# Performance work log

Hardware: AMD Instinct MI355X
Metric: run time of the kernel (lower is better)

Reference implementation:

```python
import jax, jax.numpy as jnp
import numpy as np

DIM = 256
HEADS = 8
WS = 7


def _ln(x, w, b, eps=1e-5):
    m = x.mean(-1, keepdims=True)
    v = x.var(-1, keepdims=True)
    return (x - m) / jnp.sqrt(v + eps) * w + b


def setup_inputs() -> dict:
    key = jax.random.key(0)
    ks = jax.random.split(key, 6)
    d = DIM
    s = 0.02
    return {
        "x": jax.random.normal(ks[0], (8, d, 224, 224), jnp.float32),
        "norm1_w": jnp.ones((d,), jnp.float32),
        "norm1_b": jnp.zeros((d,), jnp.float32),
        "in_proj_w": jax.random.normal(ks[1], (3 * d, d), jnp.float32) * s,
        "in_proj_b": jnp.zeros((3 * d,), jnp.float32),
        "out_proj_w": jax.random.normal(ks[2], (d, d), jnp.float32) * s,
        "out_proj_b": jnp.zeros((d,), jnp.float32),
        "norm2_w": jnp.ones((d,), jnp.float32),
        "norm2_b": jnp.zeros((d,), jnp.float32),
        "mlp_w1": jax.random.normal(ks[3], (4 * d, d), jnp.float32) * s,
        "mlp_b1": jnp.zeros((4 * d,), jnp.float32),
        "mlp_w2": jax.random.normal(ks[4], (d, 4 * d), jnp.float32) * s,
        "mlp_b2": jnp.zeros((d,), jnp.float32),
    }


def reference(x, norm1_w, norm1_b, in_proj_w, in_proj_b, out_proj_w, out_proj_b,
              norm2_w, norm2_b, mlp_w1, mlp_b1, mlp_w2, mlp_b2):
    B, C, H, W = x.shape
    ws, h = WS, HEADS
    dh = C // h
    pad_h = (ws - H % ws) % ws
    pad_w = (ws - W % ws) % ws
    xp = jnp.pad(x, ((0, 0), (0, 0), (0, pad_h), (0, pad_w)))
    Hp, Wp = xp.shape[2], xp.shape[3]
    # window partition: (B,C,Hp,Wp) -> (B*nWh*nWw, ws*ws, C)
    win = xp.reshape(B, C, Hp // ws, ws, Wp // ws, ws)
    win = win.transpose(0, 2, 4, 3, 5, 1).reshape(-1, ws * ws, C)
    win = _ln(win, norm1_w, norm1_b)  # residual stream is the NORMED windows (as in source)
    # multi-head self-attention (torch nn.MultiheadAttention semantics)
    qkv = win @ in_proj_w.T + in_proj_b
    q, k, v = jnp.split(qkv, 3, axis=-1)
    N, L, _ = win.shape
    q = q.reshape(N, L, h, dh)
    k = k.reshape(N, L, h, dh)
    v = v.reshape(N, L, h, dh)
    scores = jnp.einsum('nlhd,nmhd->nhlm', q, k) / jnp.sqrt(jnp.float32(dh))
    att = jax.nn.softmax(scores, axis=-1)
    o = jnp.einsum('nhlm,nmhd->nlhd', att, v).reshape(N, L, C)
    o = o @ out_proj_w.T + out_proj_b
    win = win + o
    # MLP with exact GELU (torch nn.GELU default)
    hmid = jax.nn.gelu(_ln(win, norm2_w, norm2_b) @ mlp_w1.T + mlp_b1, approximate=False)
    win = win + (hmid @ mlp_w2.T + mlp_b2)
    # window reverse: (N, ws*ws, C) -> (B, C, Hp, Wp)
    xo = win.reshape(B, Hp // ws, Wp // ws, ws, ws, C)
    xo = xo.transpose(0, 5, 1, 3, 2, 4).reshape(B, C, Hp, Wp)
    return xo[:, :, :H, :W]
```

## Files before the change

### kernel.cpp

```cpp
#include <hip/hip_runtime.h>
#include <hip/hip_bf16.h>
#include <math.h>

#define DEVI __device__ __forceinline__
typedef __attribute__((ext_vector_type(8))) short bf16x8;
typedef __attribute__((ext_vector_type(4))) float f32x4;

#define MFMA(a, b, c) __builtin_amdgcn_mfma_f32_16x16x32_bf16((a), (b), (c), 0, 0, 0)

DEVI short f2bf(float f) {
    unsigned u = __builtin_bit_cast(unsigned, f);
    return (short)((u + 0x7FFFu + ((u >> 16) & 1u)) >> 16);
}
DEVI float bf2f(short s) {
    unsigned u = ((unsigned)(unsigned short)s) << 16;
    return __builtin_bit_cast(float, u);
}
DEVI int swz(int row, int cb, int ld) { return row * ld + (cb ^ ((row & 7) << 4)); }
DEVI bf16x8 gload_bf8(const float* p) {
    const f32x4* q = (const f32x4*)p;
    f32x4 a = q[0], b = q[1];
    bf16x8 r;
    r[0] = f2bf(a[0]); r[1] = f2bf(a[1]); r[2] = f2bf(a[2]); r[3] = f2bf(a[3]);
    r[4] = f2bf(b[0]); r[5] = f2bf(b[1]); r[6] = f2bf(b[2]); r[7] = f2bf(b[3]);
    return r;
}

__global__ void prep_frag(const float* __restrict__ s, short* __restrict__ d,
                          int kd32, int n) {
    int i = blockIdx.x * 256 + threadIdx.x;
    if (i >= n) return;
    int lane = i & 63;
    int gt = i >> 6;
    int g = gt % kd32, tile = gt / kd32;
    int j = tile * 16 + (lane & 15);
    int k0 = g * 32 + (lane >> 4) * 8;
    int Kd = kd32 * 32;
    bf16x8 o = gload_bf8(s + (size_t)j * Kd + k0);
    *(bf16x8*)(d + (size_t)i * 8) = o;
}

__global__ __launch_bounds__(512, 2) void swin_attn(
    const float* __restrict__ x,
    const float* __restrict__ n1w, const float* __restrict__ n1b,
    const short* __restrict__ WqB, const float* __restrict__ Bq,
    const short* __restrict__ WoB, const float* __restrict__ Bo,
    short* __restrict__ Rws)
{
    extern __shared__ __align__(16) char smem[];
    constexpr int OB = 0, CQ = 25088, CK = 31360, CV = 37632, SW = 50176, ST = 75264;

    const int bid = blockIdx.x;
    const int b = bid >> 10, wh = (bid >> 5) & 31, w7 = bid & 31;
    const int tid = threadIdx.x, wv = tid >> 6, lane = tid & 63;
    const int lg = lane >> 4, l15 = lane & 15;
    const int c0 = wv * 32 + l15;
    const f32x4 z = {0.f, 0.f, 0.f, 0.f};

    {
        float* sX = (float*)smem;
        const float* xb = x + (size_t)b * (256 * 224 * 224);
        for (int i = tid; i < 256 * 49; i += 512) {
            int c = i / 49, l = i - c * 49;
            int hh = wh * 7 + l / 7, ww = w7 * 7 + (l % 7);
            sX[i] = xb[((size_t)c * 224 + hh) * 224 + ww];
        }
    }
    __syncthreads();
    {
        const int l = tid >> 3, s = tid & 7;
        if (l < 49) {
            const float* sX = (const float*)smem;
            float sum = 0.f, sq = 0.f;
            for (int ii = 0; ii < 32; ++ii) {
                int c = s * 32 + ((ii + tid) & 31);
                float v = sX[c * 49 + l];
                sum += v; sq += v * v;
            }
#pragma unroll
            for (int m = 1; m < 8; m <<= 1) { sum += __shfl_xor(sum, m); sq += __shfl_xor(sq, m); }
            if (s == 0) {
                float mean = sum * (1.f / 256.f);
                ((float*)(smem + ST))[l * 2] = mean;
                ((float*)(smem + ST))[l * 2 + 1] = rsqrtf(sq * (1.f / 256.f) - mean * mean + 1e-5f);
            }
        }
    }
    __syncthreads();
    {
        const float* sX = (const float*)smem;
        const float* st = (const float*)(smem + ST);
        float w0 = n1w[c0], b0 = n1b[c0], w1 = n1w[c0 + 16], b1 = n1b[c0 + 16];
#pragma unroll
        for (int ct = 0; ct < 2; ++ct)
#pragma unroll
        for (int mt = 0; mt < 4; ++mt)
#pragma unroll
        for (int r = 0; r < 4; ++r) {
            int row = mt * 16 + lg * 4 + r, col = c0 + ct * 16;
            if (row < 49) {
                float v = (sX[col * 49 + row] - st[row * 2]) * st[row * 2 + 1] * (ct ? w1 : w0) + (ct ? b1 : b0);
                *(short*)(smem + SW + swz(row, col * 2, 512)) = f2bf(v);
            }
        }
    }
    __syncthreads();

    const int grp = wv >> 2, mts = wv & 3;
    int arow = mts * 16 + l15; if (arow > 48) arow = 48;
#pragma unroll 1
    for (int hp = 0; hp < 4; ++hp) {
#pragma unroll 1
        for (int sub = 0; sub < 2; ++sub) {
            if (sub == 0 || wv < 4) {
                const int t = sub ? (8 + wv) : wv;
                const int part = t >> 2, tt = t & 3;
                const int lc = tt * 16 + l15;
                const int jw = part * 256 + hp * 64 + lc;
                const int wtile = part * 16 + hp * 4 + tt;
                f32x4 a0 = z, a1 = z, a2 = z, a3 = z;
#pragma unroll
                for (int kk = 0; kk < 8; ++kk) {
                    bf16x8 bw = *(const bf16x8*)(WqB + (((size_t)(wtile * 8 + kk) * 64 + lane) << 3));
                    const int cb = kk * 64 + lg * 16;
                    bf16x8 f0 = *(const bf16x8*)(smem + SW + swz(l15, cb, 512));
                    bf16x8 f1 = *(const bf16x8*)(smem + SW + swz(16 + l15, cb, 512));
                    bf16x8 f2 = *(const bf16x8*)(smem + SW + swz(32 + l15, cb, 512));
                    bf16x8 f3 = *(const bf16x8*)(smem + SW + swz(48, cb, 512));
                    a0 = MFMA(f0, bw, a0); a1 = MFMA(f1, bw, a1);
                    a2 = MFMA(f2, bw, a2); a3 = MFMA(f3, bw, a3);
                }
                const float bias = Bq[jw];
                if (part < 2) {
                    char* base = smem + (part ? CK : CQ);
#pragma unroll
                    for (int mt = 0; mt < 4; ++mt) {
                        f32x4 av = (mt == 0) ? a0 : (mt == 1) ? a1 : (mt == 2) ? a2 : a3;
#pragma unroll
                        for (int r = 0; r < 4; ++r) {
                            int row = mt * 16 + lg * 4 + r;
                            if (row < 49) *(short*)(base + swz(row, lc * 2, 128)) = f2bf(av[r] + bias);
                        }
                    }
                } else {
#pragma unroll
                    for (int mt = 0; mt < 4; ++mt) {
                        f32x4 av = (mt == 0) ? a0 : (mt == 1) ? a1 : (mt == 2) ? a2 : a3;
#pragma unroll
                        for (int r = 0; r < 4; ++r) {
                            int row = mt * 16 + lg * 4 + r;
                            *(short*)(smem + CV + swz(lc, row * 2, 128)) = f2bf(av[r] + bias);
                        }
                    }
                }
            }
        }
        __syncthreads();
        const int hb = grp * 64 + lg * 16;
        f32x4 s0 = z, s1 = z, s2 = z, s3 = z;
        {
            bf16x8 qa = *(const bf16x8*)(smem + CQ + swz(arow, hb, 128));
            bf16x8 k0 = *(const bf16x8*)(smem + CK + swz(l15, hb, 128));
            bf16x8 k1 = *(const bf16x8*)(smem + CK + swz(16 + l15, hb, 128));
            bf16x8 k2 = *(const bf16x8*)(smem + CK + swz(32 + l15, hb, 128));
            bf16x8 k3 = *(const bf16x8*)(smem + CK + swz(48, hb, 128));
            s0 = MFMA(qa, k0, s0); s1 = MFMA(qa, k1, s1);
            s2 = MFMA(qa, k2, s2); s3 = MFMA(qa, k3, s3);
        }
        const float scale = 0.17677669529663687f;
        float pr[4][4];
#pragma unroll
        for (int rj = 0; rj < 4; ++rj) {
            float v0 = s0[rj] * scale, v1 = s1[rj] * scale;
            float v2 = s2[rj] * scale, v3 = s3[rj] * scale;
            const int c3 = 48 + l15;
            float mx = fmaxf(fmaxf(v0, v1), v2);
            if (c3 < 49) mx = fmaxf(mx, v3);
#pragma unroll
            for (int mm = 1; mm < 16; mm <<= 1) mx = fmaxf(mx, __shfl_xor(mx, mm));
            float e0 = __expf(v0 - mx), e1 = __expf(v1 - mx), e2 = __expf(v2 - mx);
            float e3 = (c3 < 49) ? __expf(v3 - mx) : 0.f;
            float sm = e0 + e1 + e2 + e3;
#pragma unroll
            for (int mm = 1; mm < 16; mm <<= 1) sm += __shfl_xor(sm, mm);
            float inv = 1.f / sm;
            pr[rj][0] = e0 * inv; pr[rj][1] = e1 * inv;
            pr[rj][2] = e2 * inv; pr[rj][3] = e3 * inv;
        }
        __syncthreads();
        char* satt = smem + CQ + grp * 6272;
#pragma unroll
        for (int rj = 0; rj < 4; ++rj) {
            int row = mts * 16 + lg * 4 + rj;
            if (row < 49) {
                *(short*)(satt + swz(row, l15 * 2, 128)) = f2bf(pr[rj][0]);
                *(short*)(satt + swz(row, (16 + l15) * 2, 128)) = f2bf(pr[rj][1]);
                *(short*)(satt + swz(row, (32 + l15) * 2, 128)) = f2bf(pr[rj][2]);
                *(short*)(satt + swz(row, (48 + l15) * 2, 128)) = f2bf(pr[rj][3]);
            }
        }
        __syncthreads();
        f32x4 o0 = z, o1 = z;
#pragma unroll
        for (int kk = 0; kk < 2; ++kk) {
            const int kb = kk * 64 + lg * 16;
            bf16x8 pa  = *(const bf16x8*)(satt + swz(arow, kb, 128));
            bf16x8 vb0 = *(const bf16x8*)(smem + CV + swz(grp * 32 + l15, kb, 128));
            bf16x8 vb1 = *(const bf16x8*)(smem + CV + swz(grp * 32 + 16 + l15, kb, 128));
            o0 = MFMA(pa, vb0, o0); o1 = MFMA(pa, vb1, o1);
        }
#pragma unroll
        for (int nt = 0; nt < 2; ++nt) {
            f32x4 ov = nt ? o1 : o0;
#pragma unroll
            for (int r = 0; r < 4; ++r) {
                int row = mts * 16 + lg * 4 + r;
                if (row < 49) {
                    int col = hp * 64 + grp * 32 + nt * 16 + l15;
                    *(short*)(smem + OB + swz(row, col * 2, 512)) = f2bf(ov[r]);
                }
            }
        }
        __syncthreads();
    }

#pragma unroll 1
    for (int ct = 0; ct < 2; ++ct) {
        const int j = c0 + ct * 16;
        const int wtile = wv * 2 + ct;
        f32x4 a0 = z, a1 = z, a2 = z, a3 = z;
#pragma unroll
        for (int kk = 0; kk < 8; ++kk) {
            bf16x8 bw = *(const bf16x8*)(WoB + (((size_t)(wtile * 8 + kk) * 64 + lane) << 3));
            const int cb = kk * 64 + lg * 16;
            bf16x8 f0 = *(const bf16x8*)(smem + OB + swz(l15, cb, 512));
            bf16x8 f1 = *(const bf16x8*)(smem + OB + swz(16 + l15, cb, 512));
            bf16x8 f2 = *(const bf16x8*)(smem + OB + swz(32 + l15, cb, 512));
            bf16x8 f3 = *(const bf16x8*)(smem + OB + swz(48, cb, 512));
            a0 = MFMA(f0, bw, a0); a1 = MFMA(f1, bw, a1);
            a2 = MFMA(f2, bw, a2); a3 = MFMA(f3, bw, a3);
        }
        const float bias = Bo[j];
#pragma unroll
        for (int mt = 0; mt < 4; ++mt) {
            f32x4 av = (mt == 0) ? a0 : (mt == 1) ? a1 : (mt == 2) ? a2 : a3;
#pragma unroll
            for (int r = 0; r < 4; ++r) {
                int row = mt * 16 + lg * 4 + r;
                if (row < 49) {
                    short* p = (short*)(smem + SW + swz(row, j * 2, 512));
                    *p = f2bf(bf2f(*p) + av[r] + bias);
                }
            }
        }
    }
    __syncthreads();
    {
        for (int i = tid; i < 49 * 32; i += 512) {
            int row = i >> 5, c8 = (i & 31) * 8;
            bf16x8 v = *(const bf16x8*)(smem + SW + swz(row, c8 * 2, 512));
            *(bf16x8*)(Rws + ((size_t)bid * 49 + row) * 256 + c8) = v;
        }
    }
}

__global__ __launch_bounds__(1024, 1) void mlp_kernel(
    const short* __restrict__ Rws,
    const float* __restrict__ n2w, const float* __restrict__ n2b,
    const short* __restrict__ W1B, const float* __restrict__ B1,
    const short* __restrict__ W2B, const float* __restrict__ B2,
    float* __restrict__ out)
{
    extern __shared__ __align__(16) char smem[];
    constexpr int HB = 65536;
    const int tile = blockIdx.x;
    const int tid = threadIdx.x, wv = tid >> 6, lane = tid & 63;
    const int lg = lane >> 4, l15 = lane & 15;
    const int wm = wv >> 3, wn = wv & 7;
    const int r0 = wm * 64;
    const f32x4 z = {0.f, 0.f, 0.f, 0.f};

#pragma unroll
    for (int it = 0; it < 4; ++it) {
        int e = it * 1024 + tid;
        int row = e >> 5, c8 = (e & 31) * 8;
        bf16x8 v = *(const bf16x8*)(Rws + ((size_t)tile * 128 + row) * 256 + c8);
        *(bf16x8*)(smem + swz(row, c8 * 2, 512)) = v;
    }
    __syncthreads();
    {
        const int row = tid >> 3, sub = tid & 7;
        bf16x8 vv[4];
        float sum = 0.f, sq = 0.f;
#pragma unroll
        for (int ii = 0; ii < 4; ++ii) {
            vv[ii] = *(const bf16x8*)(smem + swz(row, (sub * 32 + ii * 8) * 2, 512));
#pragma unroll
            for (int j = 0; j < 8; ++j) { float f = bf2f(vv[ii][j]); sum += f; sq += f * f; }
        }
#pragma unroll
        for (int m = 1; m < 8; m <<= 1) { sum += __shfl_xor(sum, m); sq += __shfl_xor(sq, m); }
        const float mean = sum * (1.f / 256.f);
        const float rstd = rsqrtf(sq * (1.f / 256.f) - mean * mean + 1e-5f);
#pragma unroll
        for (int ii = 0; ii < 4; ++ii) {
            f32x4 w0 = *(const f32x4*)(n2w + sub * 32 + ii * 8);
            f32x4 w1 = *(const f32x4*)(n2w + sub * 32 + ii * 8 + 4);
            f32x4 b0 = *(const f32x4*)(n2b + sub * 32 + ii * 8);
            f32x4 b1 = *(const f32x4*)(n2b + sub * 32 + ii * 8 + 4);
            bf16x8 o;
#pragma unroll
            for (int j = 0; j < 8; ++j) {
                float wj = (j < 4) ? w0[j] : w1[j - 4];
                float bj = (j < 4) ? b0[j] : b1[j - 4];
                o[j] = f2bf((bf2f(vv[ii][j]) - mean) * rstd * wj + bj);
            }
            *(bf16x8*)(smem + swz(row, (sub * 32 + ii * 8) * 2, 512)) = o;
        }
    }
    __syncthreads();

    f32x4 macc[8];
#pragma unroll
    for (int i = 0; i < 8; ++i) macc[i] = z;

#pragma unroll 1
    for (int c = 0; c < 8; ++c) {
        f32x4 g1[4];
#pragma unroll
        for (int i = 0; i < 4; ++i) g1[i] = z;
#pragma unroll
        for (int kk = 0; kk < 8; ++kk) {
            const int cb = kk * 64 + lg * 16;
            bf16x8 a0 = *(const bf16x8*)(smem + swz(r0 + l15,      cb, 512));
            bf16x8 a1 = *(const bf16x8*)(smem + swz(r0 + 16 + l15, cb, 512));
            bf16x8 a2 = *(const bf16x8*)(smem + swz(r0 + 32 + l15, cb, 512));
            bf16x8 a3 = *(const bf16x8*)(smem + swz(r0 + 48 + l15, cb, 512));
            const int t = c * 8 + wn;
            bf16x8 wf = *(const bf16x8*)(W1B + (((size_t)(t * 8 + kk) * 64 + lane) << 3));
            g1[0] = MFMA(a0, wf, g1[0]);
            g1[1] = MFMA(a1, wf, g1[1]);
            g1[2] = MFMA(a2, wf, g1[2]);
            g1[3] = MFMA(a3, wf, g1[3]);
        }
        __syncthreads();
        {
            const int hc = wn * 16 + l15;
            const float bias = B1[c * 128 + hc];
#pragma unroll
            for (int mt = 0; mt < 4; ++mt) {
#pragma unroll
                for (int r = 0; r < 4; ++r) {
                    int row = r0 + mt * 16 + lg * 4 + r;
                    float v = g1[mt][r] + bias;
                    float g = v / (1.f + __expf(-v * (1.595769122f + 0.071354816f * v * v)));
                    *(short*)(smem + HB + swz(row, hc * 2, 256)) = f2bf(g);
                }
            }
        }
        __syncthreads();
#pragma unroll
        for (int ks = 0; ks < 4; ++ks) {
            const int cb = ks * 64 + lg * 16;
            bf16x8 h0 = *(const bf16x8*)(smem + HB + swz(r0 + l15,      cb, 256));
            bf16x8 h1 = *(const bf16x8*)(smem + HB + swz(r0 + 16 + l15, cb, 256));
            bf16x8 h2 = *(const bf16x8*)(smem + HB + swz(r0 + 32 + l15, cb, 256));
            bf16x8 h3 = *(const bf16x8*)(smem + HB + swz(r0 + 48 + l15, cb, 256));
#pragma unroll
            for (int ct = 0; ct < 2; ++ct) {
                const int t = wn * 2 + ct;
                const int g = c * 4 + ks;
                bf16x8 wf = *(const bf16x8*)(W2B + (((size_t)(t * 32 + g) * 64 + lane) << 3));
                macc[ct * 4 + 0] = MFMA(h0, wf, macc[ct * 4 + 0]);
                macc[ct * 4 + 1] = MFMA(h1, wf, macc[ct * 4 + 1]);
                macc[ct * 4 + 2] = MFMA(h2, wf, macc[ct * 4 + 2]);
                macc[ct * 4 + 3] = MFMA(h3, wf, macc[ct * 4 + 3]);
            }
        }
    }
    __syncthreads();
    float* stg = (float*)smem;
#pragma unroll 1
    for (int half = 0; half < 2; ++half) {
        if (wm == half) {
#pragma unroll
            for (int ct = 0; ct < 2; ++ct) {
                const int col = wn * 32 + ct * 16 + l15;
                const float b2v = B2[col];
#pragma unroll
                for (int mt = 0; mt < 4; ++mt) {
#pragma unroll
                    for (int r = 0; r < 4; ++r) {
                        int rl = mt * 16 + lg * 4 + r;
                        size_t t = (size_t)tile * 128 + half * 64 + rl;
                        float rv = bf2f(Rws[t * 256 + col]);
                        stg[rl * 260 + col] = rv + macc[ct * 4 + mt][r] + b2v;
                    }
                }
            }
        }
        __syncthreads();
        for (int i = tid; i < 64 * 256; i += 1024) {
            int cc = i >> 6, rl = i & 63;
            int t = tile * 128 + half * 64 + rl;
            int win = t / 49, l = t - win * 49;
            int b = win >> 10, wh = (win >> 5) & 31, w7 = win & 31;
            out[((size_t)(b * 256 + cc) * 224 + wh * 7 + l / 7) * 224 + w7 * 7 + (l % 7)] =
                stg[rl * 260 + cc];
        }
        __syncthreads();
    }
}

extern "C" void kernel_launch(void* const* d_in, const int* in_sizes, int n_in,
                              void* d_out, int out_size, void* d_ws, size_t ws_size,
                              hipStream_t stream) {
    const float* x   = (const float*)d_in[0];
    const float* n1w = (const float*)d_in[1];
    const float* n1b = (const float*)d_in[2];
    const float* Wq  = (const float*)d_in[3];
    const float* Bq  = (const float*)d_in[4];
    const float* Wo  = (const float*)d_in[5];
    const float* Bo  = (const float*)d_in[6];
    const float* n2w = (const float*)d_in[7];
    const float* n2b = (const float*)d_in[8];
    const float* W1  = (const float*)d_in[9];
    const float* B1  = (const float*)d_in[10];
    const float* W2  = (const float*)d_in[11];
    const float* B2  = (const float*)d_in[12];
    float* out = (float*)d_out;
    (void)in_sizes; (void)n_in; (void)out_size; (void)ws_size;

    short* wsp = (short*)d_ws;
    short* WqF = wsp;
    short* WoF = wsp + 196608;
    short* W1F = wsp + 262144;
    short* W2F = wsp + 524288;
    short* Rws = wsp + 786432;

    prep_frag<<<96, 256, 0, stream>>>(Wq, WqF, 8, 24576);
    prep_frag<<<32, 256, 0, stream>>>(Wo, WoF, 8, 8192);
    prep_frag<<<128, 256, 0, stream>>>(W1, W1F, 8, 32768);
    prep_frag<<<128, 256, 0, stream>>>(W2, W2F, 32, 32768);

    swin_attn<<<8192, 512, 76288, stream>>>(x, n1w, n1b, WqF, Bq, WoF, Bo, Rws);
    mlp_kernel<<<3136, 1024, 98304, stream>>>(Rws, n2w, n2b, W1F, B1, W2F, B2, out);
}
```

Baseline: 2.253 ms.

## Rebalance QKV work across waves, drop attention barriers, double MLP hidden chunk

In the attention kernel, QKV projection work is redistributed so all 8 waves do one Q/K tile plus half a V tile, replacing the two-pass schedule where only half the waves ran the second pass. The attention probabilities move to a separate per-group area in OB, which removes two __syncthreads per head pair. The outputs for the last two head pairs are kept in registers and written after the loop. The MLP kernel processes 256-wide hidden chunks in 4 iterations instead of 128-wide in 8, halving the barriers there. That costs more shared memory (131072 bytes) and accumulator registers, which may reduce occupancy.

```diff
diff --git a/kernel.cpp b/kernel.cpp
--- a/kernel.cpp
+++ b/kernel.cpp
@@ -108,50 +108,63 @@
 
     const int grp = wv >> 2, mts = wv & 3;
     int arow = mts * 16 + l15; if (arow > 48) arow = 48;
+    char* satt = smem + OB + 256 + grp * 128;
+    f32x4 osave[4];
+
 #pragma unroll 1
     for (int hp = 0; hp < 4; ++hp) {
-#pragma unroll 1
-        for (int sub = 0; sub < 2; ++sub) {
-            if (sub == 0 || wv < 4) {
-                const int t = sub ? (8 + wv) : wv;
-                const int part = t >> 2, tt = t & 3;
-                const int lc = tt * 16 + l15;
-                const int jw = part * 256 + hp * 64 + lc;
-                const int wtile = part * 16 + hp * 4 + tt;
-                f32x4 a0 = z, a1 = z, a2 = z, a3 = z;
-#pragma unroll
-                for (int kk = 0; kk < 8; ++kk) {
-                    bf16x8 bw = *(const bf16x8*)(WqB + (((size_t)(wtile * 8 + kk) * 64 + lane) << 3));
-                    const int cb = kk * 64 + lg * 16;
-                    bf16x8 f0 = *(const bf16x8*)(smem + SW + swz(l15, cb, 512));
-                    bf16x8 f1 = *(const bf16x8*)(smem + SW + swz(16 + l15, cb, 512));
-                    bf16x8 f2 = *(const bf16x8*)(smem + SW + swz(32 + l15, cb, 512));
-                    bf16x8 f3 = *(const bf16x8*)(smem + SW + swz(48, cb, 512));
-                    a0 = MFMA(f0, bw, a0); a1 = MFMA(f1, bw, a1);
-                    a2 = MFMA(f2, bw, a2); a3 = MFMA(f3, bw, a3);
-                }
-                const float bias = Bq[jw];
-                if (part < 2) {
-                    char* base = smem + (part ? CK : CQ);
-#pragma unroll
-                    for (int mt = 0; mt < 4; ++mt) {
-                        f32x4 av = (mt == 0) ? a0 : (mt == 1) ? a1 : (mt == 2) ? a2 : a3;
-#pragma unroll
-                        for (int r = 0; r < 4; ++r) {
-                            int row = mt * 16 + lg * 4 + r;
-                            if (row < 49) *(short*)(base + swz(row, lc * 2, 128)) = f2bf(av[r] + bias);
-                        }
-                    }
-                } else {
-#pragma unroll
-                    for (int mt = 0; mt < 4; ++mt) {
-                        f32x4 av = (mt == 0) ? a0 : (mt == 1) ? a1 : (mt == 2) ? a2 : a3;
-#pragma unroll
-                        for (int r = 0; r < 4; ++r) {
-                            int row = mt * 16 + lg * 4 + r;
-                            *(short*)(smem + CV + swz(lc, row * 2, 128)) = f2bf(av[r] + bias);
-                        }
-                    }
+        {
+            const int part = wv >> 2, tt = wv & 3;
+            const int lc = tt * 16 + l15;
+            const int jw = part * 256 + hp * 64 + lc;
+            const int wtile = part * 16 + hp * 4 + tt;
+            f32x4 a0 = z, a1 = z, a2 = z, a3 = z;
+#pragma unroll
+            for (int kk = 0; kk < 8; ++kk) {
+                bf16x8 bw = *(const bf16x8*)(WqB + (((size_t)(wtile * 8 + kk) * 64 + lane) << 3));
+                const int cb = kk * 64 + lg * 16;
+                bf16x8 f0 = *(const bf16x8*)(smem + SW + swz(l15, cb, 512));
+                bf16x8 f1 = *(const bf16x8*)(smem + SW + swz(16 + l15, cb, 512));
+                bf16x8 f2 = *(const bf16x8*)(smem + SW + swz(32 + l15, cb, 512));
+                bf16x8 f3 = *(const bf16x8*)(smem + SW + swz(48, cb, 512));
+                a0 = MFMA(f0, bw, a0); a1 = MFMA(f1, bw, a1);
+                a2 = MFMA(f2, bw, a2); a3 = MFMA(f3, bw, a3);
+            }
+            const float bias = Bq[jw];
+            char* base = smem + (part ? CK : CQ);
+#pragma unroll
+            for (int mt = 0; mt < 4; ++mt) {
+                f32x4 av = (mt == 0) ? a0 : (mt == 1) ? a1 : (mt == 2) ? a2 : a3;
+#pragma unroll
+                for (int r = 0; r < 4; ++r) {
+                    int row = mt * 16 + lg * 4 + r;
+                    if (row < 49) *(short*)(base + swz(row, lc * 2, 128)) = f2bf(av[r] + bias);
+                }
+            }
+        }
+        {
+            const int tt = wv & 3, hf = wv >> 2;
+            const int lc = tt * 16 + l15;
+            const int jw = 512 + hp * 64 + lc;
+            const int wtile = 32 + hp * 4 + tt;
+            f32x4 a0 = z, a1 = z;
+#pragma unroll
+            for (int kk = 0; kk < 8; ++kk) {
+                bf16x8 bw = *(const bf16x8*)(WqB + (((size_t)(wtile * 8 + kk) * 64 + lane) << 3));
+                const int cb = kk * 64 + lg * 16;
+                bf16x8 f0 = *(const bf16x8*)(smem + SW + swz(hf * 32 + l15, cb, 512));
+                bf16x8 f1 = hf ? *(const bf16x8*)(smem + SW + swz(48, cb, 512))
+                               : *(const bf16x8*)(smem + SW + swz(16 + l15, cb, 512));
+                a0 = MFMA(f0, bw, a0); a1 = MFMA(f1, bw, a1);
+            }
+            const float bias = Bq[jw];
+#pragma unroll
+            for (int mt = 0; mt < 2; ++mt) {
+                f32x4 av = mt ? a1 : a0;
+#pragma unroll
+                for (int r = 0; r < 4; ++r) {
+                    int row = (hf * 2 + mt) * 16 + lg * 4 + r;
+                    *(short*)(smem + CV + swz(lc, row * 2, 128)) = f2bf(av[r] + bias);
                 }
             }
         }
@@ -168,7 +181,6 @@
             s2 = MFMA(qa, k2, s2); s3 = MFMA(qa, k3, s3);
         }
         const float scale = 0.17677669529663687f;
-        float pr[4][4];
 #pragma unroll
         for (int rj = 0; rj < 4; ++rj) {
             float v0 = s0[rj] * scale, v1 = s1[rj] * scale;
@@ -184,45 +196,55 @@
 #pragma unroll
             for (int mm = 1; mm < 16; mm <<= 1) sm += __shfl_xor(sm, mm);
             float inv = 1.f / sm;
-            pr[rj][0] = e0 * inv; pr[rj][1] = e1 * inv;
-            pr[rj][2] = e2 * inv; pr[rj][3] = e3 * inv;
-        }
-        __syncthreads();
-        char* satt = smem + CQ + grp * 6272;
-#pragma unroll
-        for (int rj = 0; rj < 4; ++rj) {
             int row = mts * 16 + lg * 4 + rj;
             if (row < 49) {
-                *(short*)(satt + swz(row, l15 * 2, 128)) = f2bf(pr[rj][0]);
-                *(short*)(satt + swz(row, (16 + l15) * 2, 128)) = f2bf(pr[rj][1]);
-                *(short*)(satt + swz(row, (32 + l15) * 2, 128)) = f2bf(pr[rj][2]);
-                *(short*)(satt + swz(row, (48 + l15) * 2, 128)) = f2bf(pr[rj][3]);
-            }
-        }
-        __syncthreads();
+                *(short*)(satt + swz(row, l15 * 2, 512)) = f2bf(e0 * inv);
+                *(short*)(satt + swz(row, (16 + l15) * 2, 512)) = f2bf(e1 * inv);
+                *(short*)(satt + swz(row, (32 + l15) * 2, 512)) = f2bf(e2 * inv);
+                *(short*)(satt + swz(row, (48 + l15) * 2, 512)) = f2bf(e3 * inv);
+            }
+        }
         f32x4 o0 = z, o1 = z;
 #pragma unroll
         for (int kk = 0; kk < 2; ++kk) {
             const int kb = kk * 64 + lg * 16;
-            bf16x8 pa  = *(const bf16x8*)(satt + swz(arow, kb, 128));
+            bf16x8 pa  = *(const bf16x8*)(satt + swz(arow, kb, 512));
             bf16x8 vb0 = *(const bf16x8*)(smem + CV + swz(grp * 32 + l15, kb, 128));
             bf16x8 vb1 = *(const bf16x8*)(smem + CV + swz(grp * 32 + 16 + l15, kb, 128));
             o0 = MFMA(pa, vb0, o0); o1 = MFMA(pa, vb1, o1);
         }
-#pragma unroll
-        for (int nt = 0; nt < 2; ++nt) {
-            f32x4 ov = nt ? o1 : o0;
-#pragma unroll
-            for (int r = 0; r < 4; ++r) {
-                int row = mts * 16 + lg * 4 + r;
-                if (row < 49) {
-                    int col = hp * 64 + grp * 32 + nt * 16 + l15;
-                    *(short*)(smem + OB + swz(row, col * 2, 512)) = f2bf(ov[r]);
-                }
-            }
-        }
-        __syncthreads();
-    }
+        if (hp < 2) {
+#pragma unroll
+            for (int nt = 0; nt < 2; ++nt) {
+                f32x4 ov = nt ? o1 : o0;
+#pragma unroll
+                for (int r = 0; r < 4; ++r) {
+                    int row = mts * 16 + lg * 4 + r;
+                    if (row < 49) {
+                        int col = hp * 64 + grp * 32 + nt * 16 + l15;
+                        *(short*)(smem + OB + swz(row, col * 2, 512)) = f2bf(ov[r]);
+                    }
+                }
+            }
+        } else if (hp == 2) { osave[0] = o0; osave[1] = o1; }
+        else                { osave[2] = o0; osave[3] = o1; }
+        __syncthreads();
+    }
+#pragma unroll
+    for (int h2 = 0; h2 < 2; ++h2)
+#pragma unroll
+    for (int nt = 0; nt < 2; ++nt) {
+        f32x4 ov = osave[h2 * 2 + nt];
+#pragma unroll
+        for (int r = 0; r < 4; ++r) {
+            int row = mts * 16 + lg * 4 + r;
+            if (row < 49) {
+                int col = (2 + h2) * 64 + grp * 32 + nt * 16 + l15;
+                *(short*)(smem + OB + swz(row, col * 2, 512)) = f2bf(ov[r]);
+            }
+        }
+    }
+    __syncthreads();
 
 #pragma unroll 1
     for (int ct = 0; ct < 2; ++ct) {
@@ -325,10 +347,10 @@
     for (int i = 0; i < 8; ++i) macc[i] = z;
 
 #pragma unroll 1
-    for (int c = 0; c < 8; ++c) {
-        f32x4 g1[4];
-#pragma unroll
-        for (int i = 0; i < 4; ++i) g1[i] = z;
+    for (int c = 0; c < 4; ++c) {
+        f32x4 g1[8];
+#pragma unroll
+        for (int i = 0; i < 8; ++i) g1[i] = z;
 #pragma unroll
         for (int kk = 0; kk < 8; ++kk) {
             const int cb = kk * 64 + lg * 16;
@@ -336,41 +358,45 @@
             bf16x8 a1 = *(const bf16x8*)(smem + swz(r0 + 16 + l15, cb, 512));
             bf16x8 a2 = *(const bf16x8*)(smem + swz(r0 + 32 + l15, cb, 512));
             bf16x8 a3 = *(const bf16x8*)(smem + swz(r0 + 48 + l15, cb, 512));
-            const int t = c * 8 + wn;
-            bf16x8 wf = *(const bf16x8*)(W1B + (((size_t)(t * 8 + kk) * 64 + lane) << 3));
-            g1[0] = MFMA(a0, wf, g1[0]);
-            g1[1] = MFMA(a1, wf, g1[1]);
-            g1[2] = MFMA(a2, wf, g1[2]);
-            g1[3] = MFMA(a3, wf, g1[3]);
-        }
-        __syncthreads();
-        {
-            const int hc = wn * 16 + l15;
-            const float bias = B1[c * 128 + hc];
+#pragma unroll
+            for (int ct = 0; ct < 2; ++ct) {
+                const int t = c * 16 + wn * 2 + ct;
+                bf16x8 wf = *(const bf16x8*)(W1B + (((size_t)(t * 8 + kk) * 64 + lane) << 3));
+                g1[ct * 4 + 0] = MFMA(a0, wf, g1[ct * 4 + 0]);
+                g1[ct * 4 + 1] = MFMA(a1, wf, g1[ct * 4 + 1]);
+                g1[ct * 4 + 2] = MFMA(a2, wf, g1[ct * 4 + 2]);
+                g1[ct * 4 + 3] = MFMA(a3, wf, g1[ct * 4 + 3]);
+            }
+        }
+        __syncthreads();
+#pragma unroll
+        for (int ct = 0; ct < 2; ++ct) {
+            const int hc = wn * 32 + ct * 16 + l15;
+            const float bias = B1[c * 256 + hc];
 #pragma unroll
             for (int mt = 0; mt < 4; ++mt) {
 #pragma unroll
                 for (int r = 0; r < 4; ++r) {
                     int row = r0 + mt * 16 + lg * 4 + r;
-                    float v = g1[mt][r] + bias;
+                    float v = g1[ct * 4 + mt][r] + bias;
                     float g = v / (1.f + __expf(-v * (1.595769122f + 0.071354816f * v * v)));
-                    *(short*)(smem + HB + swz(row, hc * 2, 256)) = f2bf(g);
-                }
-            }
-        }
-        __syncthreads();
-#pragma unroll
-        for (int ks = 0; ks < 4; ++ks) {
+                    *(short*)(smem + HB + swz(row, hc * 2, 512)) = f2bf(g);
+                }
+            }
+        }
+        __syncthreads();
+#pragma unroll
+        for (int ks = 0; ks < 8; ++ks) {
             const int cb = ks * 64 + lg * 16;
-            bf16x8 h0 = *(const bf16x8*)(smem + HB + swz(r0 + l15,      cb, 256));
-            bf16x8 h1 = *(const bf16x8*)(smem + HB + swz(r0 + 16 + l15, cb, 256));
-            bf16x8 h2 = *(const bf16x8*)(smem + HB + swz(r0 + 32 + l15, cb, 256));
-            bf16x8 h3 = *(const bf16x8*)(smem + HB + swz(r0 + 48 + l15, cb, 256));
+            bf16x8 h0 = *(const bf16x8*)(smem + HB + swz(r0 + l15,      cb, 512));
+            bf16x8 h1 = *(const bf16x8*)(smem + HB + swz(r0 + 16 + l15, cb, 512));
+            bf16x8 h2 = *(const bf16x8*)(smem + HB + swz(r0 + 32 + l15, cb, 512));
+            bf16x8 h3 = *(const bf16x8*)(smem + HB + swz(r0 + 48 + l15, cb, 512));
 #pragma unroll
             for (int ct = 0; ct < 2; ++ct) {
-                const int t = wn * 2 + ct;
-                const int g = c * 4 + ks;
-                bf16x8 wf = *(const bf16x8*)(W2B + (((size_t)(t * 32 + g) * 64 + lane) << 3));
+                const int t2 = wn * 2 + ct;
+                const int g = c * 8 + ks;
+                bf16x8 wf = *(const bf16x8*)(W2B + (((size_t)(t2 * 32 + g) * 64 + lane) << 3));
                 macc[ct * 4 + 0] = MFMA(h0, wf, macc[ct * 4 + 0]);
                 macc[ct * 4 + 1] = MFMA(h1, wf, macc[ct * 4 + 1]);
                 macc[ct * 4 + 2] = MFMA(h2, wf, macc[ct * 4 + 2]);
@@ -444,5 +470,5 @@
     prep_frag<<<128, 256, 0, stream>>>(W2, W2F, 32, 32768);
 
     swin_attn<<<8192, 512, 76288, stream>>>(x, n1w, n1b, WqF, Bq, WoF, Bo, Rws);
-    mlp_kernel<<<3136, 1024, 98304, stream>>>(Rws, n2w, n2b, W1F, B1, W2F, B2, out);
-}
+    mlp_kernel<<<3136, 1024, 131072, stream>>>(Rws, n2w, n2b, W1F, B1, W2F, B2, out);
+}
```

Result: slower. 2.991 ms (+32.7%).

## Double-buffer MLP hidden tile and widen LDS swizzle for 512-byte rows

Applied to the files above, without the earlier changes.

The MLP hidden-activation buffer alternates between two LDS regions by chunk parity. This lets the barrier between the first GEMM and the GELU write be removed, since writers no longer overwrite data other waves may still be reading. The XOR swizzle for 512- and 256-byte row buffers now uses 16 row phases instead of 8, to cut LDS bank conflicts on the wide fragment loads. The MLP kernel's dynamic LDS grows from 96 KB to 128 KB, which may lower occupancy.

```diff
diff --git a/kernel.cpp b/kernel.cpp
--- a/kernel.cpp
+++ b/kernel.cpp
@@ -16,7 +16,8 @@
     unsigned u = ((unsigned)(unsigned short)s) << 16;
     return __builtin_bit_cast(float, u);
 }
-DEVI int swz(int row, int cb, int ld) { return row * ld + (cb ^ ((row & 7) << 4)); }
+DEVI int swz8(int row, int cb, int ld) { return row * ld + (cb ^ ((row & 7) << 4)); }
+DEVI int swz16(int row, int cb, int ld) { return row * ld + (cb ^ ((row & 15) << 4)); }
 DEVI bf16x8 gload_bf8(const float* p) {
     const f32x4* q = (const f32x4*)p;
     f32x4 a = q[0], b = q[1];
@@ -100,7 +101,7 @@
             int row = mt * 16 + lg * 4 + r, col = c0 + ct * 16;
             if (row < 49) {
                 float v = (sX[col * 49 + row] - st[row * 2]) * st[row * 2 + 1] * (ct ? w1 : w0) + (ct ? b1 : b0);
-                *(short*)(smem + SW + swz(row, col * 2, 512)) = f2bf(v);
+                *(short*)(smem + SW + swz16(row, col * 2, 512)) = f2bf(v);
             }
         }
     }
@@ -123,10 +124,10 @@
                 for (int kk = 0; kk < 8; ++kk) {
                     bf16x8 bw = *(const bf16x8*)(WqB + (((size_t)(wtile * 8 + kk) * 64 + lane) << 3));
                     const int cb = kk * 64 + lg * 16;
-                    bf16x8 f0 = *(const bf16x8*)(smem + SW + swz(l15, cb, 512));
-                    bf16x8 f1 = *(const bf16x8*)(smem + SW + swz(16 + l15, cb, 512));
-                    bf16x8 f2 = *(const bf16x8*)(smem + SW + swz(32 + l15, cb, 512));
-                    bf16x8 f3 = *(const bf16x8*)(smem + SW + swz(48, cb, 512));
+                    bf16x8 f0 = *(const bf16x8*)(smem + SW + swz16(l15, cb, 512));
+                    bf16x8 f1 = *(const bf16x8*)(smem + SW + swz16(16 + l15, cb, 512));
+                    bf16x8 f2 = *(const bf16x8*)(smem + SW + swz16(32 + l15, cb, 512));
+                    bf16x8 f3 = *(const bf16x8*)(smem + SW + swz16(48, cb, 512));
                     a0 = MFMA(f0, bw, a0); a1 = MFMA(f1, bw, a1);
                     a2 = MFMA(f2, bw, a2); a3 = MFMA(f3, bw, a3);
                 }
@@ -139,7 +140,7 @@
 #pragma unroll
                         for (int r = 0; r < 4; ++r) {
                             int row = mt * 16 + lg * 4 + r;
-                            if (row < 49) *(short*)(base + swz(row, lc * 2, 128)) = f2bf(av[r] + bias);
+                            if (row < 49) *(short*)(base + swz8(row, lc * 2, 128)) = f2bf(av[r] + bias);
                         }
                     }
                 } else {
@@ -149,7 +150,7 @@
 #pragma unroll
                         for (int r = 0; r < 4; ++r) {
                             int row = mt * 16 + lg * 4 + r;
-                            *(short*)(smem + CV + swz(lc, row * 2, 128)) = f2bf(av[r] + bias);
+                            *(short*)(smem + CV + swz8(lc, row * 2, 128)) = f2bf(av[r] + bias);
                         }
                     }
                 }
@@ -159,11 +160,11 @@
         const int hb = grp * 64 + lg * 16;
         f32x4 s0 = z, s1 = z, s2 = z, s3 = z;
         {
-            bf16x8 qa = *(const bf16x8*)(smem + CQ + swz(arow, hb, 128));
-            bf16x8 k0 = *(const bf16x8*)(smem + CK + swz(l15, hb, 128));
-            bf16x8 k1 = *(const bf16x8*)(smem + CK + swz(16 + l15, hb, 128));
-            bf16x8 k2 = *(const bf16x8*)(smem + CK + swz(32 + l15, hb, 128));
-            bf16x8 k3 = *(const bf16x8*)(smem + CK + swz(48, hb, 128));
+            bf16x8 qa = *(const bf16x8*)(smem + CQ + swz8(arow, hb, 128));
+            bf16x8 k0 = *(const bf16x8*)(smem + CK + swz8(l15, hb, 128));
+            bf16x8 k1 = *(const bf16x8*)(smem + CK + swz8(16 + l15, hb, 128));
+            bf16x8 k2 = *(const bf16x8*)(smem + CK + swz8(32 + l15, hb, 128));
+            bf16x8 k3 = *(const bf16x8*)(smem + CK + swz8(48, hb, 128));
             s0 = MFMA(qa, k0, s0); s1 = MFMA(qa, k1, s1);
             s2 = MFMA(qa, k2, s2); s3 = MFMA(qa, k3, s3);
         }
@@ -193,10 +194,10 @@
         for (int rj = 0; rj < 4; ++rj) {
             int row = mts * 16 + lg * 4 + rj;
             if (row < 49) {
-                *(short*)(satt + swz(row, l15 * 2, 128)) = f2bf(pr[rj][0]);
-                *(short*)(satt + swz(row, (16 + l15) * 2, 128)) = f2bf(pr[rj][1]);
-                *(short*)(satt + swz(row, (32 + l15) * 2, 128)) = f2bf(pr[rj][2]);
-                *(short*)(satt + swz(row, (48 + l15) * 2, 128)) = f2bf(pr[rj][3]);
+                *(short*)(satt + swz8(row, l15 * 2, 128)) = f2bf(pr[rj][0]);
+                *(short*)(satt + swz8(row, (16 + l15) * 2, 128)) = f2bf(pr[rj][1]);
+                *(short*)(satt + swz8(row, (32 + l15) * 2, 128)) = f2bf(pr[rj][2]);
+                *(short*)(satt + swz8(row, (48 + l15) * 2, 128)) = f2bf(pr[rj][3]);
             }
         }
         __syncthreads();
@@ -204,9 +205,9 @@
 #pragma unroll
         for (int kk = 0; kk < 2; ++kk) {
             const int kb = kk * 64 + lg * 16;
-            bf16x8 pa  = *(const bf16x8*)(satt + swz(arow, kb, 128));
-            bf16x8 vb0 = *(const bf16x8*)(smem + CV + swz(grp * 32 + l15, kb, 128));
-            bf16x8 vb1 = *(const bf16x8*)(smem + CV + swz(grp * 32 + 16 + l15, kb, 128));
+            bf16x8 pa  = *(const bf16x8*)(satt + swz8(arow, kb, 128));
+            bf16x8 vb0 = *(const bf16x8*)(smem + CV + swz8(grp * 32 + l15, kb, 128));
+            bf16x8 vb1 = *(const bf16x8*)(smem + CV + swz8(grp * 32 + 16 + l15, kb, 128));
             o0 = MFMA(pa, vb0, o0); o1 = MFMA(pa, vb1, o1);
         }
 #pragma unroll
@@ -217,7 +218,7 @@
                 int row = mts * 16 + lg * 4 + r;
                 if (row < 49) {
                     int col = hp * 64 + grp * 32 + nt * 16 + l15;
-                    *(short*)(smem + OB + swz(row, col * 2, 512)) = f2bf(ov[r]);
+                    *(short*)(smem + OB + swz16(row, col * 2, 512)) = f2bf(ov[r]);
                 }
             }
         }
@@ -233,10 +234,10 @@
         for (int kk = 0; kk < 8; ++kk) {
             bf16x8 bw = *(const bf16x8*)(WoB + (((size_t)(wtile * 8 + kk) * 64 + lane) << 3));
             const int cb = kk * 64 + lg * 16;
-            bf16x8 f0 = *(const bf16x8*)(smem + OB + swz(l15, cb, 512));
-            bf16x8 f1 = *(const bf16x8*)(smem + OB + swz(16 + l15, cb, 512));
-            bf16x8 f2 = *(const bf16x8*)(smem + OB + swz(32 + l15, cb, 512));
-            bf16x8 f3 = *(const bf16x8*)(smem + OB + swz(48, cb, 512));
+            bf16x8 f0 = *(const bf16x8*)(smem + OB + swz16(l15, cb, 512));
+            bf16x8 f1 = *(const bf16x8*)(smem + OB + swz16(16 + l15, cb, 512));
+            bf16x8 f2 = *(const bf16x8*)(smem + OB + swz16(32 + l15, cb, 512));
+            bf16x8 f3 = *(const bf16x8*)(smem + OB + swz16(48, cb, 512));
             a0 = MFMA(f0, bw, a0); a1 = MFMA(f1, bw, a1);
             a2 = MFMA(f2, bw, a2); a3 = MFMA(f3, bw, a3);
         }
@@ -248,7 +249,7 @@
             for (int r = 0; r < 4; ++r) {
                 int row = mt * 16 + lg * 4 + r;
                 if (row < 49) {
-                    short* p = (short*)(smem + SW + swz(row, j * 2, 512));
+                    short* p = (short*)(smem + SW + swz16(row, j * 2, 512));
                     *p = f2bf(bf2f(*p) + av[r] + bias);
                 }
             }
@@ -258,7 +259,7 @@
     {
         for (int i = tid; i < 49 * 32; i += 512) {
             int row = i >> 5, c8 = (i & 31) * 8;
-            bf16x8 v = *(const bf16x8*)(smem + SW + swz(row, c8 * 2, 512));
+            bf16x8 v = *(const bf16x8*)(smem + SW + swz16(row, c8 * 2, 512));
             *(bf16x8*)(Rws + ((size_t)bid * 49 + row) * 256 + c8) = v;
         }
     }
@@ -272,7 +273,7 @@
     float* __restrict__ out)
 {
     extern __shared__ __align__(16) char smem[];
-    constexpr int HB = 65536;
+    constexpr int HB0 = 65536, HB1 = 98304;
     const int tile = blockIdx.x;
     const int tid = threadIdx.x, wv = tid >> 6, lane = tid & 63;
     const int lg = lane >> 4, l15 = lane & 15;
@@ -285,7 +286,7 @@
         int e = it * 1024 + tid;
         int row = e >> 5, c8 = (e & 31) * 8;
         bf16x8 v = *(const bf16x8*)(Rws + ((size_t)tile * 128 + row) * 256 + c8);
-        *(bf16x8*)(smem + swz(row, c8 * 2, 512)) = v;
+        *(bf16x8*)(smem + swz16(row, c8 * 2, 512)) = v;
     }
     __syncthreads();
     {
@@ -294,7 +295,7 @@
         float sum = 0.f, sq = 0.f;
 #pragma unroll
         for (int ii = 0; ii < 4; ++ii) {
-            vv[ii] = *(const bf16x8*)(smem + swz(row, (sub * 32 + ii * 8) * 2, 512));
+            vv[ii] = *(const bf16x8*)(smem + swz16(row, (sub * 32 + ii * 8) * 2, 512));
 #pragma unroll
             for (int j = 0; j < 8; ++j) { float f = bf2f(vv[ii][j]); sum += f; sq += f * f; }
         }
@@ -315,7 +316,7 @@
                 float bj = (j < 4) ? b0[j] : b1[j - 4];
                 o[j] = f2bf((bf2f(vv[ii][j]) - mean) * rstd * wj + bj);
             }
-            *(bf16x8*)(smem + swz(row, (sub * 32 + ii * 8) * 2, 512)) = o;
+            *(bf16x8*)(smem + swz16(row, (sub * 32 + ii * 8) * 2, 512)) = o;
         }
     }
     __syncthreads();
@@ -326,16 +327,17 @@
 
 #pragma unroll 1
     for (int c = 0; c < 8; ++c) {
+        char* HB = smem + ((c & 1) ? HB1 : HB0);
         f32x4 g1[4];
 #pragma unroll
         for (int i = 0; i < 4; ++i) g1[i] = z;
 #pragma unroll
         for (int kk = 0; kk < 8; ++kk) {
             const int cb = kk * 64 + lg * 16;
-            bf16x8 a0 = *(const bf16x8*)(smem + swz(r0 + l15,      cb, 512));
-            bf16x8 a1 = *(const bf16x8*)(smem + swz(r0 + 16 + l15, cb, 512));
-            bf16x8 a2 = *(const bf16x8*)(smem + swz(r0 + 32 + l15, cb, 512));
-            bf16x8 a3 = *(const bf16x8*)(smem + swz(r0 + 48 + l15, cb, 512));
+            bf16x8 a0 = *(const bf16x8*)(smem + swz16(r0 + l15,      cb, 512));
+            bf16x8 a1 = *(const bf16x8*)(smem + swz16(r0 + 16 + l15, cb, 512));
+            bf16x8 a2 = *(const bf16x8*)(smem + swz16(r0 + 32 + l15, cb, 512));
+            bf16x8 a3 = *(const bf16x8*)(smem + swz16(r0 + 48 + l15, cb, 512));
             const int t = c * 8 + wn;
             bf16x8 wf = *(const bf16x8*)(W1B + (((size_t)(t * 8 + kk) * 64 + lane) << 3));
             g1[0] = MFMA(a0, wf, g1[0]);
@@ -343,7 +345,6 @@
             g1[2] = MFMA(a2, wf, g1[2]);
             g1[3] = MFMA(a3, wf, g1[3]);
         }
-        __syncthreads();
         {
             const int hc = wn * 16 + l15;
             const float bias = B1[c * 128 + hc];
@@ -354,7 +355,7 @@
                     int row = r0 + mt * 16 + lg * 4 + r;
                     float v = g1[mt][r] + bias;
                     float g = v / (1.f + __expf(-v * (1.595769122f + 0.071354816f * v * v)));
-                    *(short*)(smem + HB + swz(row, hc * 2, 256)) = f2bf(g);
+                    *(short*)(HB + swz16(row, hc * 2, 256)) = f2bf(g);
                 }
             }
         }
@@ -362,15 +363,15 @@
 #pragma unroll
         for (int ks = 0; ks < 4; ++ks) {
             const int cb = ks * 64 + lg * 16;
-            bf16x8 h0 = *(const bf16x8*)(smem + HB + swz(r0 + l15,      cb, 256));
-            bf16x8 h1 = *(const bf16x8*)(smem + HB + swz(r0 + 16 + l15, cb, 256));
-            bf16x8 h2 = *(const bf16x8*)(smem + HB + swz(r0 + 32 + l15, cb, 256));
-            bf16x8 h3 = *(const bf16x8*)(smem + HB + swz(r0 + 48 + l15, cb, 256));
+            bf16x8 h0 = *(const bf16x8*)(HB + swz16(r0 + l15,      cb, 256));
+            bf16x8 h1 = *(const bf16x8*)(HB + swz16(r0 + 16 + l15, cb, 256));
+            bf16x8 h2 = *(const bf16x8*)(HB + swz16(r0 + 32 + l15, cb, 256));
+            bf16x8 h3 = *(const bf16x8*)(HB + swz16(r0 + 48 + l15, cb, 256));
 #pragma unroll
             for (int ct = 0; ct < 2; ++ct) {
-                const int t = wn * 2 + ct;
+                const int t2 = wn * 2 + ct;
                 const int g = c * 4 + ks;
-                bf16x8 wf = *(const bf16x8*)(W2B + (((size_t)(t * 32 + g) * 64 + lane) << 3));
+                bf16x8 wf = *(const bf16x8*)(W2B + (((size_t)(t2 * 32 + g) * 64 + lane) << 3));
                 macc[ct * 4 + 0] = MFMA(h0, wf, macc[ct * 4 + 0]);
                 macc[ct * 4 + 1] = MFMA(h1, wf, macc[ct * 4 + 1]);
                 macc[ct * 4 + 2] = MFMA(h2, wf, macc[ct * 4 + 2]);
@@ -444,5 +445,5 @@
     prep_frag<<<128, 256, 0, stream>>>(W2, W2F, 32, 32768);
 
     swin_attn<<<8192, 512, 76288, stream>>>(x, n1w, n1b, WqF, Bq, WoF, Bo, Rws);
-    mlp_kernel<<<3136, 1024, 98304, stream>>>(Rws, n2w, n2b, W1F, B1, W2F, B2, out);
-}
+    mlp_kernel<<<3136, 1024, 131072, stream>>>(Rws, n2w, n2b, W1F, B1, W2F, B2, out);
+}
```

Measured after the change: 2.213 ms. Within noise of the previous version (-1.8%).
